# Kernel optimization log

Hardware: AMD Instinct MI355X
Metric: run time of the kernel (lower is better)

The kernel has to match this reference:

```python
import jax, jax.numpy as jnp
import numpy as np

BATCH, STEP, IN_DIM, HID = 16384, 5, 11, 512


def setup_inputs() -> dict:
    key = jax.random.key(0)
    k1, k2, k3, k4, k5 = jax.random.split(key, 5)
    s = 1.0 / np.sqrt(HID)  # torch LSTMCell init scale (uniform +-1/sqrt(hidden))
    return {
        "time_series": jax.random.normal(k1, (BATCH, STEP, IN_DIM), jnp.float32),
        "W_ih": jax.random.uniform(k2, (4 * HID, IN_DIM), jnp.float32, -s, s),
        "W_hh": jax.random.uniform(k3, (4 * HID, HID), jnp.float32, -s, s),
        "b_ih": jax.random.uniform(k4, (4 * HID,), jnp.float32, -s, s),
        "b_hh": jax.random.uniform(k5, (4 * HID,), jnp.float32, -s, s),
    }


def _lstm_scan(time_series, W_ih, W_hh, b_ih, b_hh):
    B = time_series.shape[0]
    H = W_hh.shape[1]
    # Precompute input projections for all steps in one big GEMM: [B, T, 4H]
    x_proj = jnp.einsum('bti,gi->btg', time_series, W_ih) + b_ih + b_hh

    def cell(carry, xg):
        h, c = carry
        gates = xg + h @ W_hh.T  # [B, 4H]
        i, f, g, o = jnp.split(gates, 4, axis=-1)  # torch gate order i,f,g,o
        i = jax.nn.sigmoid(i)
        f = jax.nn.sigmoid(f)
        g = jnp.tanh(g)
        o = jax.nn.sigmoid(o)
        c_new = f * c + i * g
        h_new = o * jnp.tanh(c_new)
        return (h_new, c_new), None

    h0 = jnp.zeros((B, H), time_series.dtype)
    c0 = jnp.zeros((B, H), time_series.dtype)
    (h, c), _ = jax.lax.scan(cell, (h0, c0), jnp.swapaxes(x_proj, 0, 1))
    return c  # original module returns the final cell state c


def reference(time_series, W_ih, W_hh, b_ih, b_hh):
    return _lstm_scan(time_series, W_ih, W_hh, b_ih, b_hh)
```

## Files before the change

kernel.cpp:

```cpp
#include <hip/hip_runtime.h>
#include <hip/hip_bf16.h>


#define HID   512
#define KSN   17
#define ROWS  64
#define NTHR  1024
#define HB    (KSN * 4 * 64 * 8)
#define SMEM_HALFS (2 * HB + 64 * 56)
#define SMEM_BYTES (SMEM_HALFS * 2)

#define L2E   1.442695041f
#define L2E2  2.885390082f

typedef _Float16 f16x8 __attribute__((ext_vector_type(8)));
typedef float f32x4 __attribute__((ext_vector_type(4)));

__global__ __launch_bounds__(256) void pack_w(const float* __restrict__ Wih,
                                              const float* __restrict__ Whh,
                                              const float* __restrict__ bih,
                                              const float* __restrict__ bhh,
                                              _Float16* __restrict__ Wt) {
    const int col  = blockIdx.x * 4 + (threadIdx.x >> 6);
    const int lane = threadIdx.x & 63;
    const int g = col >> 9;
    const int j = (col & 511) >> 4;
    const int c = col & 15;
    const float scale = (g == 2) ? L2E2 : L2E;

    const float4* __restrict__ src = (const float4*)(Whh + (size_t)col * 512);
    float4 u0 = src[lane * 2 + 0];
    float4 u1 = src[lane * 2 + 1];
    _Float16 v[8];
    v[0] = (_Float16)(u0.x * scale);
    v[1] = (_Float16)(u0.y * scale);
    v[2] = (_Float16)(u0.z * scale);
    v[3] = (_Float16)(u0.w * scale);
    v[4] = (_Float16)(u1.x * scale);
    v[5] = (_Float16)(u1.y * scale);
    v[6] = (_Float16)(u1.z * scale);
    v[7] = (_Float16)(u1.w * scale);
    const int ks = lane >> 2, kq = lane & 3;
    const size_t frag = ((size_t)j * KSN + ks) * 4 + g;
    *(f16x8*)(Wt + frag * 512 + (c + 16 * kq) * 8) = *(const f16x8*)v;

    if (lane < 4) {
        _Float16 w[8];
        const int kb = 512 + lane * 8;
#pragma unroll
        for (int q = 0; q < 8; q++) {
            int k = kb + q;
            float x;
            if (k < 523)       x = Wih[col * 11 + (k - 512)];
            else if (k == 523) x = bih[col] + bhh[col];
            else               x = 0.0f;
            w[q] = (_Float16)(x * scale);
        }
        const size_t fragt = ((size_t)j * KSN + 16) * 4 + g;
        *(f16x8*)(Wt + fragt * 512 + (c + 16 * lane) * 8) = *(const f16x8*)w;
    }
}

template <int KS0, bool WRITE_H>
__device__ __forceinline__ void run_step(const _Float16* __restrict__ cur,
                                         _Float16* __restrict__ nxt,
                                         const char* __restrict__ wbase,
                                         f32x4* __restrict__ cacc,
                                         const int wave, const int lane) {
    const int c  = lane & 15;
    const int kq = lane >> 4;
    const int lane16 = lane * 16;
#pragma unroll
    for (int ji = 0; ji < 2; ji++) {
        const int jj = __builtin_amdgcn_readfirstlane(wave * 2 + ji);
        const char* __restrict__ wjs = wbase + (size_t)jj * (KSN * 4096)
                                             + (size_t)KS0 * 4096;
        const char* __restrict__ ac = (const char*)cur + KS0 * 4096 + lane16;

        f32x4 acc[4][4];
#pragma unroll
        for (int rt = 0; rt < 4; rt++)
#pragma unroll
            for (int g = 0; g < 4; g++) {
                f32x4 z = {0.f, 0.f, 0.f, 0.f};
                acc[rt][g] = z;
            }

#pragma unroll 1
        for (int ks = KS0; ks < KSN; ks++) {
            f16x8 B0 = *(const f16x8*)(wjs + lane16 + 0);
            f16x8 B1 = *(const f16x8*)(wjs + lane16 + 1024);
            f16x8 B2 = *(const f16x8*)(wjs + lane16 + 2048);
            f16x8 B3 = *(const f16x8*)(wjs + lane16 + 3072);
#pragma unroll
            for (int rt = 0; rt < 4; rt++) {
                f16x8 A = *(const f16x8*)(ac + rt * 1024);
                acc[rt][0] = __builtin_amdgcn_mfma_f32_16x16x32_f16(A, B0, acc[rt][0], 0, 0, 0);
                acc[rt][1] = __builtin_amdgcn_mfma_f32_16x16x32_f16(A, B1, acc[rt][1], 0, 0, 0);
                acc[rt][2] = __builtin_amdgcn_mfma_f32_16x16x32_f16(A, B2, acc[rt][2], 0, 0, 0);
                acc[rt][3] = __builtin_amdgcn_mfma_f32_16x16x32_f16(A, B3, acc[rt][3], 0, 0, 0);
            }
            wjs += 4096;
            ac  += 4096;
        }

        const int j = wave * 2 + ji;
        _Float16* __restrict__ hw = nxt + (j >> 1) * 2048
            + (kq * 4 + 16 * (((j & 1) << 1) | (c >> 3))) * 8 + (c & 7);
#pragma unroll
        for (int rt = 0; rt < 4; rt++) {
            f32x4 cv = cacc[ji * 4 + rt];
#pragma unroll
            for (int r = 0; r < 4; r++) {
                float ai = acc[rt][0][r];
                float af = acc[rt][1][r];
                float ag = acc[rt][2][r];
                float ao = acc[rt][3][r];
                float ei = __builtin_amdgcn_exp2f(-ai);
                float eg = __builtin_amdgcn_exp2f(ag);
                float ig = (eg - 1.0f) *
                           __builtin_amdgcn_rcpf((1.0f + ei) * (1.0f + eg));
                float ef = __builtin_amdgcn_exp2f(-af);
                float cn = __builtin_amdgcn_rcpf(1.0f + ef) * cv[r] + ig;
                cv[r] = cn;
                if (WRITE_H) {
                    float eo = __builtin_amdgcn_exp2f(-ao);
                    float ec = __builtin_amdgcn_exp2f(cn * L2E2);
                    float hn = (ec - 1.0f) *
                               __builtin_amdgcn_rcpf((1.0f + eo) * (1.0f + ec));
                    hw[rt * 512 + r * 8] = (_Float16)hn;
                }
            }
            cacc[ji * 4 + rt] = cv;
        }
    }
}

__device__ __forceinline__ void xfill(_Float16* __restrict__ nxt,
                                      const _Float16* __restrict__ xlds,
                                      int step, int tid) {
    for (int i = tid; i < 64 * 11; i += NTHR) {
        int row = i / 11, xi = i - row * 11;
        int idx = ((16 * 4 + (row >> 4)) * 64 + ((row & 15) + 16 * (xi >> 3))) * 8
                  + (xi & 7);
        nxt[idx] = xlds[row * 56 + step * 11 + xi];
    }
}

__global__ __launch_bounds__(NTHR, 4)
void lstm_main(const float* __restrict__ ts,
               const _Float16* __restrict__ Wt,
               float* __restrict__ out) {
    extern __shared__ _Float16 smem[];
    _Float16* buf0 = smem;
    _Float16* buf1 = smem + HB;
    _Float16* xlds = smem + 2 * HB;
    const int tid  = threadIdx.x;
    const int lane = tid & 63;
    const int wave = tid >> 6;
    const int b0   = blockIdx.x * ROWS;
    const char* wbase = (const char*)Wt;

    {
        f16x8 z = {(_Float16)0, (_Float16)0, (_Float16)0, (_Float16)0,
                   (_Float16)0, (_Float16)0, (_Float16)0, (_Float16)0};
        for (int i = tid * 8; i < 2 * HB; i += NTHR * 8)
            *(f16x8*)(smem + i) = z;
    }
    for (int i = tid; i < 64 * 55; i += NTHR) {
        int row = i / 55, e = i - row * 55;
        xlds[row * 56 + e] = (_Float16)ts[(size_t)(b0 + row) * 55 + e];
    }
    __syncthreads();
    if (tid < 128) {
        int bsel = tid >> 6, row = tid & 63;
        int idx = ((16 * 4 + (row >> 4)) * 64 + ((row & 15) + 16)) * 8 + 3;
        (bsel ? buf1 : buf0)[idx] = (_Float16)1.0f;
    }
    xfill(buf0, xlds, 0, tid);
    __syncthreads();

    f32x4 cacc[8];
#pragma unroll
    for (int i = 0; i < 8; i++) {
        f32x4 z = {0.f, 0.f, 0.f, 0.f};
        cacc[i] = z;
    }

    run_step<16, true>(buf0, buf1, wbase, cacc, wave, lane);
    xfill(buf1, xlds, 1, tid);
    __syncthreads();

    for (int t = 1; t < 4; t++) {
        _Float16* cur = (t & 1) ? buf1 : buf0;
        _Float16* nxt = (t & 1) ? buf0 : buf1;
        run_step<0, true>(cur, nxt, wbase, cacc, wave, lane);
        xfill(nxt, xlds, t + 1, tid);
        __syncthreads();
    }
    run_step<0, false>(buf0, buf1, wbase, cacc, wave, lane);

    const int c = lane & 15, kq = lane >> 4;
#pragma unroll
    for (int ji = 0; ji < 2; ji++) {
        const int j = wave * 2 + ji;
#pragma unroll
        for (int rt = 0; rt < 4; rt++) {
            f32x4 cv = cacc[ji * 4 + rt];
#pragma unroll
            for (int r = 0; r < 4; r++)
                out[(size_t)(b0 + rt * 16 + kq * 4 + r) * HID + j * 16 + c] = cv[r];
        }
    }
}

extern "C" void kernel_launch(void* const* d_in, const int* in_sizes, int n_in,
                              void* d_out, int out_size, void* d_ws, size_t ws_size,
                              hipStream_t stream) {
    const float* ts  = (const float*)d_in[0];
    const float* Wih = (const float*)d_in[1];
    const float* Whh = (const float*)d_in[2];
    const float* bih = (const float*)d_in[3];
    const float* bhh = (const float*)d_in[4];
    float* out       = (float*)d_out;
    _Float16* Wt     = (_Float16*)d_ws;

    (void)in_sizes; (void)n_in; (void)out_size; (void)ws_size;

    hipFuncSetAttribute(reinterpret_cast<const void*>(lstm_main),
                        hipFuncAttributeMaxDynamicSharedMemorySize, SMEM_BYTES);

    pack_w<<<512, 256, 0, stream>>>(Wih, Whh, bih, bhh, Wt);
    lstm_main<<<256, NTHR, SMEM_BYTES, stream>>>(ts, Wt, out);
}
```

Before: 208.7 us.

## Fuse weight packing into LSTM kernel via cooperative launch and grid sync

Folds the weight-packing pre-pass into the main LSTM kernel: each of the 256 blocks packs 8 gate columns with its first 8 waves, then a cooperative grid-wide sync replaces the block barrier before the recurrence. This removes one kernel launch and the gap between the two kernels. It also raises wave priority around the MFMA inner loop. In exchange it needs a cooperative launch, and all 256 blocks must be co-resident for the grid sync. The grid barrier itself adds a cost.

After: 248.9 us. 1.19x slower.

```diff
diff --git a/kernel.cpp b/kernel.cpp
--- a/kernel.cpp
+++ b/kernel.cpp
@@ -1,5 +1,8 @@
 #include <hip/hip_runtime.h>
 #include <hip/hip_bf16.h>
+#include <hip/hip_cooperative_groups.h>
+
+namespace cg = cooperative_groups;
 
 
 #define HID   512
@@ -16,13 +19,12 @@
 typedef _Float16 f16x8 __attribute__((ext_vector_type(8)));
 typedef float f32x4 __attribute__((ext_vector_type(4)));
 
-__global__ __launch_bounds__(256) void pack_w(const float* __restrict__ Wih,
-                                              const float* __restrict__ Whh,
-                                              const float* __restrict__ bih,
-                                              const float* __restrict__ bhh,
-                                              _Float16* __restrict__ Wt) {
-    const int col  = blockIdx.x * 4 + (threadIdx.x >> 6);
-    const int lane = threadIdx.x & 63;
+__device__ __forceinline__ void pack_col(const int col, const int lane,
+                                         const float* __restrict__ Wih,
+                                         const float* __restrict__ Whh,
+                                         const float* __restrict__ bih,
+                                         const float* __restrict__ bhh,
+                                         _Float16* __restrict__ Wt) {
     const int g = col >> 9;
     const int j = (col & 511) >> 4;
     const int c = col & 15;
@@ -92,6 +94,7 @@
             f16x8 B1 = *(const f16x8*)(wjs + lane16 + 1024);
             f16x8 B2 = *(const f16x8*)(wjs + lane16 + 2048);
             f16x8 B3 = *(const f16x8*)(wjs + lane16 + 3072);
+            __builtin_amdgcn_s_setprio(1);
 #pragma unroll
             for (int rt = 0; rt < 4; rt++) {
                 f16x8 A = *(const f16x8*)(ac + rt * 1024);
@@ -100,6 +103,7 @@
                 acc[rt][2] = __builtin_amdgcn_mfma_f32_16x16x32_f16(A, B2, acc[rt][2], 0, 0, 0);
                 acc[rt][3] = __builtin_amdgcn_mfma_f32_16x16x32_f16(A, B3, acc[rt][3], 0, 0, 0);
             }
+            __builtin_amdgcn_s_setprio(0);
             wjs += 4096;
             ac  += 4096;
         }
@@ -148,9 +152,13 @@
 }
 
 __global__ __launch_bounds__(NTHR, 4)
-void lstm_main(const float* __restrict__ ts,
-               const _Float16* __restrict__ Wt,
-               float* __restrict__ out) {
+void lstm_fused(const float* __restrict__ ts,
+                const float* __restrict__ Wih,
+                const float* __restrict__ Whh,
+                const float* __restrict__ bih,
+                const float* __restrict__ bhh,
+                _Float16* __restrict__ Wt,
+                float* __restrict__ out) {
     extern __shared__ _Float16 smem[];
     _Float16* buf0 = smem;
     _Float16* buf1 = smem + HB;
@@ -161,6 +169,9 @@
     const int b0   = blockIdx.x * ROWS;
     const char* wbase = (const char*)Wt;
 
+    if (wave < 8)
+        pack_col(blockIdx.x * 8 + wave, lane, Wih, Whh, bih, bhh, Wt);
+
     {
         f16x8 z = {(_Float16)0, (_Float16)0, (_Float16)0, (_Float16)0,
                    (_Float16)0, (_Float16)0, (_Float16)0, (_Float16)0};
@@ -178,7 +189,8 @@
         (bsel ? buf1 : buf0)[idx] = (_Float16)1.0f;
     }
     xfill(buf0, xlds, 0, tid);
-    __syncthreads();
+
+    cg::this_grid().sync();
 
     f32x4 cacc[8];
 #pragma unroll
@@ -227,9 +239,12 @@
 
     (void)in_sizes; (void)n_in; (void)out_size; (void)ws_size;
 
-    hipFuncSetAttribute(reinterpret_cast<const void*>(lstm_main),
+    hipFuncSetAttribute(reinterpret_cast<const void*>(lstm_fused),
                         hipFuncAttributeMaxDynamicSharedMemorySize, SMEM_BYTES);
 
-    pack_w<<<512, 256, 0, stream>>>(Wih, Whh, bih, bhh, Wt);
-    lstm_main<<<256, NTHR, SMEM_BYTES, stream>>>(ts, Wt, out);
-}
+    void* args[] = {(void*)&ts, (void*)&Wih, (void*)&Whh, (void*)&bih,
+                    (void*)&bhh, (void*)&Wt, (void*)&out};
+    hipLaunchCooperativeKernel(reinterpret_cast<const void*>(lstm_fused),
+                               dim3(256), dim3(NTHR), args,
+                               (unsigned)SMEM_BYTES, stream);
+}
```

## Halve block threads and give each wave four column tiles with shared A loads

Applied to the files above, without the earlier changes.

The block drops from 16 to 8 waves, so each wave now handles four 16-column hidden tiles instead of two. It processes them in two passes, each computing two tiles at once so every A fragment read from LDS feeds 32 MFMAs instead of 16. This is meant to cut LDS traffic for the h operand and raise MFMA density per load. The cost is a larger accumulator footprint (128 fp32 acc values plus 64 cell-state values per lane), higher register pressure, and half as many waves resident to hide latency.

Result: slower. 218.9 us (+4.9%).

```diff
diff --git a/kernel.cpp b/kernel.cpp
--- a/kernel.cpp
+++ b/kernel.cpp
@@ -5,7 +5,7 @@
 #define HID   512
 #define KSN   17
 #define ROWS  64
-#define NTHR  1024
+#define NTHR  512
 #define HB    (KSN * 4 * 64 * 8)
 #define SMEM_HALFS (2 * HB + 64 * 56)
 #define SMEM_BYTES (SMEM_HALFS * 2)
@@ -61,8 +61,8 @@
     }
 }
 
-template <int KS0, bool WRITE_H>
-__device__ __forceinline__ void run_step(const _Float16* __restrict__ cur,
+template <int KS0, int PP, bool WRITE_H>
+__device__ __forceinline__ void run_pass(const _Float16* __restrict__ cur,
                                          _Float16* __restrict__ nxt,
                                          const char* __restrict__ wbase,
                                          f32x4* __restrict__ cacc,
@@ -70,52 +70,65 @@
     const int c  = lane & 15;
     const int kq = lane >> 4;
     const int lane16 = lane * 16;
-#pragma unroll
-    for (int ji = 0; ji < 2; ji++) {
-        const int jj = __builtin_amdgcn_readfirstlane(wave * 2 + ji);
-        const char* __restrict__ wjs = wbase + (size_t)jj * (KSN * 4096)
-                                             + (size_t)KS0 * 4096;
-        const char* __restrict__ ac = (const char*)cur + KS0 * 4096 + lane16;
-
-        f32x4 acc[4][4];
+
+    const int jj0 = __builtin_amdgcn_readfirstlane(wave * 4 + PP * 2);
+    const char* __restrict__ w0 = wbase + (size_t)jj0 * (KSN * 4096)
+                                        + (size_t)KS0 * 4096;
+    const char* __restrict__ w1 = w0 + (size_t)(KSN * 4096);
+    const char* __restrict__ ac = (const char*)cur + KS0 * 4096 + lane16;
+
+    f32x4 acc[2][4][4];
+#pragma unroll
+    for (int ji = 0; ji < 2; ji++)
 #pragma unroll
         for (int rt = 0; rt < 4; rt++)
 #pragma unroll
             for (int g = 0; g < 4; g++) {
                 f32x4 z = {0.f, 0.f, 0.f, 0.f};
-                acc[rt][g] = z;
+                acc[ji][rt][g] = z;
             }
 
 #pragma unroll 1
-        for (int ks = KS0; ks < KSN; ks++) {
-            f16x8 B0 = *(const f16x8*)(wjs + lane16 + 0);
-            f16x8 B1 = *(const f16x8*)(wjs + lane16 + 1024);
-            f16x8 B2 = *(const f16x8*)(wjs + lane16 + 2048);
-            f16x8 B3 = *(const f16x8*)(wjs + lane16 + 3072);
-#pragma unroll
-            for (int rt = 0; rt < 4; rt++) {
-                f16x8 A = *(const f16x8*)(ac + rt * 1024);
-                acc[rt][0] = __builtin_amdgcn_mfma_f32_16x16x32_f16(A, B0, acc[rt][0], 0, 0, 0);
-                acc[rt][1] = __builtin_amdgcn_mfma_f32_16x16x32_f16(A, B1, acc[rt][1], 0, 0, 0);
-                acc[rt][2] = __builtin_amdgcn_mfma_f32_16x16x32_f16(A, B2, acc[rt][2], 0, 0, 0);
-                acc[rt][3] = __builtin_amdgcn_mfma_f32_16x16x32_f16(A, B3, acc[rt][3], 0, 0, 0);
-            }
-            wjs += 4096;
-            ac  += 4096;
-        }
-
-        const int j = wave * 2 + ji;
+    for (int ks = KS0; ks < KSN; ks++) {
+        f16x8 B00 = *(const f16x8*)(w0 + lane16 + 0);
+        f16x8 B01 = *(const f16x8*)(w0 + lane16 + 1024);
+        f16x8 B02 = *(const f16x8*)(w0 + lane16 + 2048);
+        f16x8 B03 = *(const f16x8*)(w0 + lane16 + 3072);
+        f16x8 B10 = *(const f16x8*)(w1 + lane16 + 0);
+        f16x8 B11 = *(const f16x8*)(w1 + lane16 + 1024);
+        f16x8 B12 = *(const f16x8*)(w1 + lane16 + 2048);
+        f16x8 B13 = *(const f16x8*)(w1 + lane16 + 3072);
+#pragma unroll
+        for (int rt = 0; rt < 4; rt++) {
+            f16x8 A = *(const f16x8*)(ac + rt * 1024);
+            acc[0][rt][0] = __builtin_amdgcn_mfma_f32_16x16x32_f16(A, B00, acc[0][rt][0], 0, 0, 0);
+            acc[0][rt][1] = __builtin_amdgcn_mfma_f32_16x16x32_f16(A, B01, acc[0][rt][1], 0, 0, 0);
+            acc[0][rt][2] = __builtin_amdgcn_mfma_f32_16x16x32_f16(A, B02, acc[0][rt][2], 0, 0, 0);
+            acc[0][rt][3] = __builtin_amdgcn_mfma_f32_16x16x32_f16(A, B03, acc[0][rt][3], 0, 0, 0);
+            acc[1][rt][0] = __builtin_amdgcn_mfma_f32_16x16x32_f16(A, B10, acc[1][rt][0], 0, 0, 0);
+            acc[1][rt][1] = __builtin_amdgcn_mfma_f32_16x16x32_f16(A, B11, acc[1][rt][1], 0, 0, 0);
+            acc[1][rt][2] = __builtin_amdgcn_mfma_f32_16x16x32_f16(A, B12, acc[1][rt][2], 0, 0, 0);
+            acc[1][rt][3] = __builtin_amdgcn_mfma_f32_16x16x32_f16(A, B13, acc[1][rt][3], 0, 0, 0);
+        }
+        w0 += 4096;
+        w1 += 4096;
+        ac += 4096;
+    }
+
+#pragma unroll
+    for (int ji = 0; ji < 2; ji++) {
+        const int j = wave * 4 + PP * 2 + ji;
         _Float16* __restrict__ hw = nxt + (j >> 1) * 2048
             + (kq * 4 + 16 * (((j & 1) << 1) | (c >> 3))) * 8 + (c & 7);
 #pragma unroll
         for (int rt = 0; rt < 4; rt++) {
-            f32x4 cv = cacc[ji * 4 + rt];
+            f32x4 cv = cacc[(PP * 2 + ji) * 4 + rt];
 #pragma unroll
             for (int r = 0; r < 4; r++) {
-                float ai = acc[rt][0][r];
-                float af = acc[rt][1][r];
-                float ag = acc[rt][2][r];
-                float ao = acc[rt][3][r];
+                float ai = acc[ji][rt][0][r];
+                float af = acc[ji][rt][1][r];
+                float ag = acc[ji][rt][2][r];
+                float ao = acc[ji][rt][3][r];
                 float ei = __builtin_amdgcn_exp2f(-ai);
                 float eg = __builtin_amdgcn_exp2f(ag);
                 float ig = (eg - 1.0f) *
@@ -131,9 +144,19 @@
                     hw[rt * 512 + r * 8] = (_Float16)hn;
                 }
             }
-            cacc[ji * 4 + rt] = cv;
-        }
-    }
+            cacc[(PP * 2 + ji) * 4 + rt] = cv;
+        }
+    }
+}
+
+template <int KS0, bool WRITE_H>
+__device__ __forceinline__ void run_step(const _Float16* __restrict__ cur,
+                                         _Float16* __restrict__ nxt,
+                                         const char* __restrict__ wbase,
+                                         f32x4* __restrict__ cacc,
+                                         const int wave, const int lane) {
+    run_pass<KS0, 0, WRITE_H>(cur, nxt, wbase, cacc, wave, lane);
+    run_pass<KS0, 1, WRITE_H>(cur, nxt, wbase, cacc, wave, lane);
 }
 
 __device__ __forceinline__ void xfill(_Float16* __restrict__ nxt,
@@ -147,7 +170,7 @@
     }
 }
 
-__global__ __launch_bounds__(NTHR, 4)
+__global__ __launch_bounds__(NTHR, 2)
 void lstm_main(const float* __restrict__ ts,
                const _Float16* __restrict__ Wt,
                float* __restrict__ out) {
@@ -180,9 +203,9 @@
     xfill(buf0, xlds, 0, tid);
     __syncthreads();
 
-    f32x4 cacc[8];
-#pragma unroll
-    for (int i = 0; i < 8; i++) {
+    f32x4 cacc[16];
+#pragma unroll
+    for (int i = 0; i < 16; i++) {
         f32x4 z = {0.f, 0.f, 0.f, 0.f};
         cacc[i] = z;
     }
@@ -202,11 +225,11 @@
 
     const int c = lane & 15, kq = lane >> 4;
 #pragma unroll
-    for (int ji = 0; ji < 2; ji++) {
-        const int j = wave * 2 + ji;
+    for (int jl = 0; jl < 4; jl++) {
+        const int j = wave * 4 + jl;
 #pragma unroll
         for (int rt = 0; rt < 4; rt++) {
-            f32x4 cv = cacc[ji * 4 + rt];
+            f32x4 cv = cacc[jl * 4 + rt];
 #pragma unroll
             for (int r = 0; r < 4; r++)
                 out[(size_t)(b0 + rt * 16 + kq * 4 + r) * HID + j * 16 + c] = cv[r];
```

## Quantize recurrent W_hh and hidden state to int8 with i8 MFMA

Applied to the files above, without the earlier changes.

Quantizes W_hh to int8 with a per-column scale and the hidden state to int8 (scaled by 127), and computes the recurrent GEMM with int8 MFMA (16x16x64). The input projection and bias stay in a separate fp16 MFMA tile. The goal is to halve weight and hidden-state bytes and use the higher int8 MFMA throughput. In exchange, h loses precision, which risks accuracy against the fp32 reference.

Measured after the change: 186.1 us, median of 2. -10.8%, faster.

```diff
diff --git a/kernel.cpp b/kernel.cpp
--- a/kernel.cpp
+++ b/kernel.cpp
@@ -3,68 +3,92 @@
 
 
 #define HID   512
-#define KSN   17
 #define ROWS  64
 #define NTHR  1024
-#define HB    (KSN * 4 * 64 * 8)
-#define SMEM_HALFS (2 * HB + 64 * 56)
+#define HBBYTES 36864
+#define HB    (HBBYTES / 2)
+#define SMEM_HALFS (2 * HB + 64 * 56 + 4096)
 #define SMEM_BYTES (SMEM_HALFS * 2)
+
+#define WT_I8   0
+#define WT_F16X 1048576
+#define WT_CSC  1179648
 
 #define L2E   1.442695041f
 #define L2E2  2.885390082f
 
 typedef _Float16 f16x8 __attribute__((ext_vector_type(8)));
 typedef float f32x4 __attribute__((ext_vector_type(4)));
+typedef int v4i __attribute__((ext_vector_type(4)));
 
 __global__ __launch_bounds__(256) void pack_w(const float* __restrict__ Wih,
                                               const float* __restrict__ Whh,
                                               const float* __restrict__ bih,
                                               const float* __restrict__ bhh,
-                                              _Float16* __restrict__ Wt) {
+                                              char* __restrict__ Wt) {
     const int col  = blockIdx.x * 4 + (threadIdx.x >> 6);
     const int lane = threadIdx.x & 63;
     const int g = col >> 9;
     const int j = (col & 511) >> 4;
     const int c = col & 15;
-    const float scale = (g == 2) ? L2E2 : L2E;
 
     const float4* __restrict__ src = (const float4*)(Whh + (size_t)col * 512);
     float4 u0 = src[lane * 2 + 0];
     float4 u1 = src[lane * 2 + 1];
-    _Float16 v[8];
-    v[0] = (_Float16)(u0.x * scale);
-    v[1] = (_Float16)(u0.y * scale);
-    v[2] = (_Float16)(u0.z * scale);
-    v[3] = (_Float16)(u0.w * scale);
-    v[4] = (_Float16)(u1.x * scale);
-    v[5] = (_Float16)(u1.y * scale);
-    v[6] = (_Float16)(u1.z * scale);
-    v[7] = (_Float16)(u1.w * scale);
-    const int ks = lane >> 2, kq = lane & 3;
-    const size_t frag = ((size_t)j * KSN + ks) * 4 + g;
-    *(f16x8*)(Wt + frag * 512 + (c + 16 * kq) * 8) = *(const f16x8*)v;
+    float w[8] = {u0.x, u0.y, u0.z, u0.w, u1.x, u1.y, u1.z, u1.w};
+
+    float m = 0.0f;
+#pragma unroll
+    for (int q = 0; q < 8; q++) m = fmaxf(m, fabsf(w[q]));
+#pragma unroll
+    for (int off = 32; off >= 1; off >>= 1)
+        m = fmaxf(m, __shfl_xor(m, off));
+    m = fmaxf(m, 1e-12f);
+    const float inv = 127.0f / m;
+
+    unsigned lo = 0, hi = 0;
+#pragma unroll
+    for (int q = 0; q < 4; q++)
+        lo |= ((unsigned)((int)rintf(w[q] * inv) & 0xff)) << (8 * q);
+#pragma unroll
+    for (int q = 0; q < 4; q++)
+        hi |= ((unsigned)((int)rintf(w[4 + q] * inv) & 0xff)) << (8 * q);
+
+    const int ks8 = lane >> 3;
+    const int p   = (lane >> 1) & 3;
+    const int bo  = (lane & 1) * 8;
+    size_t addr = ((size_t)(j * 8 + ks8) * 4 + g) * 1024 + (c + 16 * p) * 16 + bo;
+    uint2 pk = {lo, hi};
+    *(uint2*)(Wt + WT_I8 + addr) = pk;
+
+    if (lane == 0) {
+        float* csc = (float*)(Wt + WT_CSC);
+        csc[col] = (m / 16129.0f) * ((g == 2) ? L2E2 : L2E);
+    }
 
     if (lane < 4) {
-        _Float16 w[8];
-        const int kb = 512 + lane * 8;
+        const float scale = (g == 2) ? L2E2 : L2E;
+        _Float16 t[8];
+        const int kb = lane * 8;
 #pragma unroll
         for (int q = 0; q < 8; q++) {
             int k = kb + q;
             float x;
-            if (k < 523)       x = Wih[col * 11 + (k - 512)];
-            else if (k == 523) x = bih[col] + bhh[col];
-            else               x = 0.0f;
-            w[q] = (_Float16)(x * scale);
-        }
-        const size_t fragt = ((size_t)j * KSN + 16) * 4 + g;
-        *(f16x8*)(Wt + fragt * 512 + (c + 16 * lane) * 8) = *(const f16x8*)w;
-    }
-}
-
-template <int KS0, bool WRITE_H>
-__device__ __forceinline__ void run_step(const _Float16* __restrict__ cur,
-                                         _Float16* __restrict__ nxt,
+            if (k < 11)       x = Wih[col * 11 + k];
+            else if (k == 11) x = bih[col] + bhh[col];
+            else              x = 0.0f;
+            t[q] = (_Float16)(x * scale);
+        }
+        *(f16x8*)(Wt + WT_F16X + ((size_t)j * 4 + g) * 1024
+                  + (c + 16 * lane) * 16) = *(const f16x8*)t;
+    }
+}
+
+template <bool FIRST, bool WRITE_H>
+__device__ __forceinline__ void run_step(const char* __restrict__ cur,
+                                         char* __restrict__ nxt,
                                          const char* __restrict__ wbase,
+                                         const float* __restrict__ colsc,
                                          f32x4* __restrict__ cacc,
                                          const int wave, const int lane) {
     const int c  = lane & 15;
@@ -72,55 +96,92 @@
     const int lane16 = lane * 16;
 #pragma unroll
     for (int ji = 0; ji < 2; ji++) {
-        const int jj = __builtin_amdgcn_readfirstlane(wave * 2 + ji);
-        const char* __restrict__ wjs = wbase + (size_t)jj * (KSN * 4096)
-                                             + (size_t)KS0 * 4096;
-        const char* __restrict__ ac = (const char*)cur + KS0 * 4096 + lane16;
-
-        f32x4 acc[4][4];
-#pragma unroll
-        for (int rt = 0; rt < 4; rt++)
-#pragma unroll
-            for (int g = 0; g < 4; g++) {
-                f32x4 z = {0.f, 0.f, 0.f, 0.f};
-                acc[rt][g] = z;
+        const int j  = wave * 2 + ji;
+        const int jj = __builtin_amdgcn_readfirstlane(j);
+
+        f32x4 af[4][4];
+        if (!FIRST) {
+            v4i acc[4][4];
+#pragma unroll
+            for (int rt = 0; rt < 4; rt++)
+#pragma unroll
+                for (int g = 0; g < 4; g++) {
+                    v4i z = {0, 0, 0, 0};
+                    acc[rt][g] = z;
+                }
+            const char* __restrict__ w0 = wbase + (size_t)jj * 32768;
+            const char* __restrict__ ac = cur + lane16;
+#pragma unroll 1
+            for (int ks = 0; ks < 8; ks++) {
+                v4i B0 = *(const v4i*)(w0 + lane16 + 0);
+                v4i B1 = *(const v4i*)(w0 + lane16 + 1024);
+                v4i B2 = *(const v4i*)(w0 + lane16 + 2048);
+                v4i B3 = *(const v4i*)(w0 + lane16 + 3072);
+#pragma unroll
+                for (int rt = 0; rt < 4; rt++) {
+                    v4i A = *(const v4i*)(ac + rt * 1024);
+                    acc[rt][0] = __builtin_amdgcn_mfma_i32_16x16x64_i8(A, B0, acc[rt][0], 0, 0, 0);
+                    acc[rt][1] = __builtin_amdgcn_mfma_i32_16x16x64_i8(A, B1, acc[rt][1], 0, 0, 0);
+                    acc[rt][2] = __builtin_amdgcn_mfma_i32_16x16x64_i8(A, B2, acc[rt][2], 0, 0, 0);
+                    acc[rt][3] = __builtin_amdgcn_mfma_i32_16x16x64_i8(A, B3, acc[rt][3], 0, 0, 0);
+                }
+                w0 += 4096;
+                ac += 4096;
             }
-
-#pragma unroll 1
-        for (int ks = KS0; ks < KSN; ks++) {
-            f16x8 B0 = *(const f16x8*)(wjs + lane16 + 0);
-            f16x8 B1 = *(const f16x8*)(wjs + lane16 + 1024);
-            f16x8 B2 = *(const f16x8*)(wjs + lane16 + 2048);
-            f16x8 B3 = *(const f16x8*)(wjs + lane16 + 3072);
+            float s0 = colsc[0 * 512 + jj * 16 + c];
+            float s1 = colsc[1 * 512 + jj * 16 + c];
+            float s2 = colsc[2 * 512 + jj * 16 + c];
+            float s3 = colsc[3 * 512 + jj * 16 + c];
+#pragma unroll
+            for (int rt = 0; rt < 4; rt++)
+#pragma unroll
+                for (int r = 0; r < 4; r++) {
+                    af[rt][0][r] = (float)acc[rt][0][r] * s0;
+                    af[rt][1][r] = (float)acc[rt][1][r] * s1;
+                    af[rt][2][r] = (float)acc[rt][2][r] * s2;
+                    af[rt][3][r] = (float)acc[rt][3][r] * s3;
+                }
+        } else {
+#pragma unroll
+            for (int rt = 0; rt < 4; rt++)
+#pragma unroll
+                for (int g = 0; g < 4; g++) {
+                    f32x4 z = {0.f, 0.f, 0.f, 0.f};
+                    af[rt][g] = z;
+                }
+        }
+
+        {
+            const char* __restrict__ wx = wbase + WT_F16X + (size_t)jj * 4096;
+            f16x8 X0 = *(const f16x8*)(wx + lane16 + 0);
+            f16x8 X1 = *(const f16x8*)(wx + lane16 + 1024);
+            f16x8 X2 = *(const f16x8*)(wx + lane16 + 2048);
+            f16x8 X3 = *(const f16x8*)(wx + lane16 + 3072);
+            const char* __restrict__ ax = cur + 32768 + lane16;
 #pragma unroll
             for (int rt = 0; rt < 4; rt++) {
-                f16x8 A = *(const f16x8*)(ac + rt * 1024);
-                acc[rt][0] = __builtin_amdgcn_mfma_f32_16x16x32_f16(A, B0, acc[rt][0], 0, 0, 0);
-                acc[rt][1] = __builtin_amdgcn_mfma_f32_16x16x32_f16(A, B1, acc[rt][1], 0, 0, 0);
-                acc[rt][2] = __builtin_amdgcn_mfma_f32_16x16x32_f16(A, B2, acc[rt][2], 0, 0, 0);
-                acc[rt][3] = __builtin_amdgcn_mfma_f32_16x16x32_f16(A, B3, acc[rt][3], 0, 0, 0);
+                f16x8 A = *(const f16x8*)(ax + rt * 1024);
+                af[rt][0] = __builtin_amdgcn_mfma_f32_16x16x32_f16(A, X0, af[rt][0], 0, 0, 0);
+                af[rt][1] = __builtin_amdgcn_mfma_f32_16x16x32_f16(A, X1, af[rt][1], 0, 0, 0);
+                af[rt][2] = __builtin_amdgcn_mfma_f32_16x16x32_f16(A, X2, af[rt][2], 0, 0, 0);
+                af[rt][3] = __builtin_amdgcn_mfma_f32_16x16x32_f16(A, X3, af[rt][3], 0, 0, 0);
             }
-            wjs += 4096;
-            ac  += 4096;
-        }
-
-        const int j = wave * 2 + ji;
-        _Float16* __restrict__ hw = nxt + (j >> 1) * 2048
-            + (kq * 4 + 16 * (((j & 1) << 1) | (c >> 3))) * 8 + (c & 7);
+        }
+
 #pragma unroll
         for (int rt = 0; rt < 4; rt++) {
             f32x4 cv = cacc[ji * 4 + rt];
 #pragma unroll
             for (int r = 0; r < 4; r++) {
-                float ai = acc[rt][0][r];
-                float af = acc[rt][1][r];
-                float ag = acc[rt][2][r];
-                float ao = acc[rt][3][r];
+                float ai = af[rt][0][r];
+                float afv = af[rt][1][r];
+                float ag = af[rt][2][r];
+                float ao = af[rt][3][r];
                 float ei = __builtin_amdgcn_exp2f(-ai);
                 float eg = __builtin_amdgcn_exp2f(ag);
                 float ig = (eg - 1.0f) *
                            __builtin_amdgcn_rcpf((1.0f + ei) * (1.0f + eg));
-                float ef = __builtin_amdgcn_exp2f(-af);
+                float ef = __builtin_amdgcn_exp2f(-afv);
                 float cn = __builtin_amdgcn_rcpf(1.0f + ef) * cv[r] + ig;
                 cv[r] = cn;
                 if (WRITE_H) {
@@ -128,7 +189,9 @@
                     float ec = __builtin_amdgcn_exp2f(cn * L2E2);
                     float hn = (ec - 1.0f) *
                                __builtin_amdgcn_rcpf((1.0f + eo) * (1.0f + ec));
-                    hw[rt * 512 + r * 8] = (_Float16)hn;
+                    int q = (int)rintf(hn * 127.0f);
+                    nxt[(((j >> 2) * 4 + rt) * 64 + (kq * 4 + r) + 16 * (j & 3)) * 16 + c]
+                        = (char)q;
                 }
             }
             cacc[ji * 4 + rt] = cv;
@@ -141,7 +204,7 @@
                                       int step, int tid) {
     for (int i = tid; i < 64 * 11; i += NTHR) {
         int row = i / 11, xi = i - row * 11;
-        int idx = ((16 * 4 + (row >> 4)) * 64 + ((row & 15) + 16 * (xi >> 3))) * 8
+        int idx = ((32 + (row >> 4)) * 64 + ((row & 15) + 16 * (xi >> 3))) * 8
                   + (xi & 7);
         nxt[idx] = xlds[row * 56 + step * 11 + xi];
     }
@@ -149,17 +212,20 @@
 
 __global__ __launch_bounds__(NTHR, 4)
 void lstm_main(const float* __restrict__ ts,
-               const _Float16* __restrict__ Wt,
+               const char* __restrict__ Wt,
                float* __restrict__ out) {
     extern __shared__ _Float16 smem[];
-    _Float16* buf0 = smem;
-    _Float16* buf1 = smem + HB;
-    _Float16* xlds = smem + 2 * HB;
+    _Float16* buf0h = smem;
+    _Float16* buf1h = smem + HB;
+    _Float16* xlds  = smem + 2 * HB;
+    float*    cslds = (float*)(smem + 2 * HB + 64 * 56);
+    char* buf0 = (char*)buf0h;
+    char* buf1 = (char*)buf1h;
     const int tid  = threadIdx.x;
     const int lane = tid & 63;
     const int wave = tid >> 6;
     const int b0   = blockIdx.x * ROWS;
-    const char* wbase = (const char*)Wt;
+    const char* wbase = Wt;
 
     {
         f16x8 z = {(_Float16)0, (_Float16)0, (_Float16)0, (_Float16)0,
@@ -171,13 +237,15 @@
         int row = i / 55, e = i - row * 55;
         xlds[row * 56 + e] = (_Float16)ts[(size_t)(b0 + row) * 55 + e];
     }
+    for (int i = tid; i < 2048; i += NTHR)
+        cslds[i] = ((const float*)(Wt + WT_CSC))[i];
     __syncthreads();
     if (tid < 128) {
         int bsel = tid >> 6, row = tid & 63;
-        int idx = ((16 * 4 + (row >> 4)) * 64 + ((row & 15) + 16)) * 8 + 3;
-        (bsel ? buf1 : buf0)[idx] = (_Float16)1.0f;
-    }
-    xfill(buf0, xlds, 0, tid);
+        int idx = ((32 + (row >> 4)) * 64 + ((row & 15) + 16)) * 8 + 3;
+        (bsel ? buf1h : buf0h)[idx] = (_Float16)1.0f;
+    }
+    xfill(buf0h, xlds, 0, tid);
     __syncthreads();
 
     f32x4 cacc[8];
@@ -187,18 +255,18 @@
         cacc[i] = z;
     }
 
-    run_step<16, true>(buf0, buf1, wbase, cacc, wave, lane);
-    xfill(buf1, xlds, 1, tid);
+    run_step<true, true>(buf0, buf1, wbase, cslds, cacc, wave, lane);
+    xfill(buf1h, xlds, 1, tid);
     __syncthreads();
 
     for (int t = 1; t < 4; t++) {
-        _Float16* cur = (t & 1) ? buf1 : buf0;
-        _Float16* nxt = (t & 1) ? buf0 : buf1;
-        run_step<0, true>(cur, nxt, wbase, cacc, wave, lane);
-        xfill(nxt, xlds, t + 1, tid);
+        char* cur = (t & 1) ? buf1 : buf0;
+        char* nxt = (t & 1) ? buf0 : buf1;
+        run_step<false, true>(cur, nxt, wbase, cslds, cacc, wave, lane);
+        xfill((t & 1) ? (_Float16*)buf0 : (_Float16*)buf1, xlds, t + 1, tid);
         __syncthreads();
     }
-    run_step<0, false>(buf0, buf1, wbase, cacc, wave, lane);
+    run_step<false, false>(buf0, buf1, wbase, cslds, cacc, wave, lane);
 
     const int c = lane & 15, kq = lane >> 4;
 #pragma unroll
@@ -223,7 +291,7 @@
     const float* bih = (const float*)d_in[3];
     const float* bhh = (const float*)d_in[4];
     float* out       = (float*)d_out;
-    _Float16* Wt     = (_Float16*)d_ws;
+    char* Wt         = (char*)d_ws;
 
     (void)in_sizes; (void)n_in; (void)out_size; (void)ws_size;
 
```
